# Performance work log

Measured on AMD Instinct MI355X. Metric: run time of the kernel, lower is better.

## Reference

```python
import jax, jax.numpy as jnp
import numpy as np

N_STEPS = 192
T_END = 8.0


def _forward(z, dec_W, dec_b, templates, def_W1, def_b1, def_W2, def_b2,
             al_W1, al_b1, al_W2, al_b2, ode_W1, ode_b1, ode_W2, ode_b2):
    B = z.shape[0]
    n_slots, crf_dim = templates.shape  # (32, 99)
    # vae.decoder: latent -> per-slot embeddings (B, 32, 64)
    slot_embs = (z @ dec_W + dec_b).reshape(B, n_slots, -1)
    # initialize_crf: template library + deformation MLP -> base CRF (B, 32, 99)
    h = jax.nn.relu(slot_embs @ def_W1 + def_b1)
    base_crf = templates[None, :, :] + (h @ def_W2 + def_b2)
    # aliveness MLP -> per-slot logits (B, 32)
    ah = jax.nn.relu(slot_embs @ al_W1 + al_b1)
    logits = (ah @ al_W2 + al_b2)[..., 0]
    alive = jax.nn.sigmoid(logits)
    # state combiner: gated CRF flattened + aliveness -> (B, 32*99 + 32) = (B, 3200)
    y0 = jnp.concatenate([(base_crf * alive[..., None]).reshape(B, -1), alive], axis=-1)

    dt = jnp.asarray(T_END / (N_STEPS - 1), y0.dtype)

    def f(y):  # ODEFx: autonomous 2-layer tanh MLP on the (B, 3200) state
        return jnp.tanh(y @ ode_W1 + ode_b1) @ ode_W2 + ode_b2

    def step(y, _):  # classic fixed-step RK4 (torchdiffeq method='rk4')
        k1 = f(y)
        k2 = f(y + 0.5 * dt * k1)
        k3 = f(y + 0.5 * dt * k2)
        k4 = f(y + dt * k3)
        yn = y + (dt / 6.0) * (k1 + 2.0 * k2 + 2.0 * k3 + k4)
        return yn, yn

    _, traj = jax.lax.scan(jax.checkpoint(step), y0, None, length=N_STEPS - 1)
    return jnp.concatenate([y0[None], traj], axis=0)  # (192, B, 3200)


def setup_inputs() -> dict:
    key = jax.random.key(0)
    ks = jax.random.split(key, 9)
    B, LAT, NS, SD, CRF, DH, OH, STATE = 128, 128, 32, 64, 99, 128, 4096, 3200
    r = lambda k, shp, fan: (jax.random.normal(k, shp, jnp.float32) / np.float32(np.sqrt(fan)))
    return dict(
        z=jax.random.normal(ks[0], (B, LAT), jnp.float32),
        dec_W=r(ks[1], (LAT, NS * SD), LAT), dec_b=jnp.zeros((NS * SD,), jnp.float32),
        templates=jax.random.normal(ks[2], (NS, CRF), jnp.float32),
        def_W1=r(ks[3], (SD, DH), SD), def_b1=jnp.zeros((DH,), jnp.float32),
        def_W2=r(ks[4], (DH, CRF), DH), def_b2=jnp.zeros((CRF,), jnp.float32),
        al_W1=r(ks[5], (SD, NS), SD), al_b1=jnp.zeros((NS,), jnp.float32),
        al_W2=r(ks[6], (NS, 1), NS), al_b2=jnp.zeros((1,), jnp.float32),
        ode_W1=r(ks[7], (STATE, OH), STATE), ode_b1=jnp.zeros((OH,), jnp.float32),
        ode_W2=r(ks[8], (OH, STATE), OH), ode_b2=jnp.zeros((STATE,), jnp.float32),
    )


def reference(z, dec_W, dec_b, templates, def_W1, def_b1, def_W2, def_b2,
              al_W1, al_b1, al_W2, al_b2, ode_W1, ode_b1, ode_W2, ode_b2):
    return _forward(z, dec_W, dec_b, templates, def_W1, def_b1, def_W2, def_b2,
                    al_W1, al_b1, al_W2, al_b2, ode_W1, ode_b1, ode_W2, ode_b2)
```

## Files before the change

### kernel.cpp

```cpp
#include <hip/hip_runtime.h>
#include <hip/hip_bf16.h>

typedef __bf16 v8bf __attribute__((ext_vector_type(8)));
typedef float  v4f  __attribute__((ext_vector_type(4)));

__device__ inline const __attribute__((address_space(1))) void* gcast(const void* p) {
    return (const __attribute__((address_space(1))) void*)p;
}
__device__ inline __attribute__((address_space(3))) void* scast(void* p) {
    return (__attribute__((address_space(3))) void*)p;
}

__device__ inline float fast_tanh(float x) {
    float e = __expf(2.0f * x);
    return 1.0f - 2.0f / (e + 1.0f);
}

__global__ __launch_bounds__(256) void se_kernel(const float* __restrict__ z,
                                                 const float* __restrict__ decW,
                                                 const float* __restrict__ decb,
                                                 float* __restrict__ SE) {
    __shared__ float zs[128];
    const int b = blockIdx.x, t = threadIdx.x;
    if (t < 128) zs[t] = z[b * 128 + t];
    __syncthreads();
    for (int c = t; c < 2048; c += 256) {
        float acc = decb[c];
        #pragma unroll 4
        for (int k = 0; k < 128; ++k) acc += zs[k] * decW[k * 2048 + c];
        SE[b * 2048 + c] = acc;
    }
}

__global__ __launch_bounds__(128) void init_kernel(
    const float* __restrict__ SE, const float* __restrict__ tmpl,
    const float* __restrict__ dW1, const float* __restrict__ db1,
    const float* __restrict__ dW2, const float* __restrict__ db2,
    const float* __restrict__ aW1, const float* __restrict__ ab1,
    const float* __restrict__ aW2, const float* __restrict__ ab2,
    float* __restrict__ y, __bf16* __restrict__ ybf, float* __restrict__ out0) {
    __shared__ float se[64];
    __shared__ float h[128];
    __shared__ float ah[32];
    __shared__ float alive;
    const int r = blockIdx.x, b = r >> 5, s = r & 31, t = threadIdx.x;
    if (t < 64) se[t] = SE[b * 2048 + s * 64 + t];
    __syncthreads();
    {
        float acc = db1[t];
        #pragma unroll 4
        for (int k = 0; k < 64; ++k) acc += se[k] * dW1[k * 128 + t];
        h[t] = fmaxf(acc, 0.0f);
    }
    if (t < 32) {
        float acc = ab1[t];
        #pragma unroll 4
        for (int k = 0; k < 64; ++k) acc += se[k] * aW1[k * 32 + t];
        ah[t] = fmaxf(acc, 0.0f);
    }
    __syncthreads();
    if (t == 0) {
        float lg = ab2[0];
        #pragma unroll
        for (int j = 0; j < 32; ++j) lg += ah[j] * aW2[j];
        alive = 1.0f / (1.0f + __expf(-lg));
    }
    __syncthreads();
    if (t < 99) {
        float acc = db2[t];
        #pragma unroll 4
        for (int j = 0; j < 128; ++j) acc += h[j] * dW2[j * 99 + t];
        float v = (tmpl[s * 99 + t] + acc) * alive;
        int idx = b * 3200 + s * 99 + t;
        y[idx] = v; ybf[idx] = (__bf16)v; out0[idx] = v;
    } else if (t == 99) {
        int idx = b * 3200 + 3168 + s;
        y[idx] = alive; ybf[idx] = (__bf16)alive; out0[idx] = alive;
    }
}

__global__ __launch_bounds__(256) void transpose_bf16(const float* __restrict__ W,
                                                      __bf16* __restrict__ WT,
                                                      int R, int C) {
    __shared__ float tile[32][33];
    const int tx = threadIdx.x & 31, ty = threadIdx.x >> 5;
    const int c0 = blockIdx.x * 32, r0 = blockIdx.y * 32;
    #pragma unroll
    for (int i = 0; i < 4; ++i)
        tile[ty + 8 * i][tx] = W[(long)(r0 + ty + 8 * i) * C + c0 + tx];
    __syncthreads();
    #pragma unroll
    for (int i = 0; i < 4; ++i)
        WT[(long)(c0 + ty + 8 * i) * R + r0 + tx] = (__bf16)tile[tx][ty + 8 * i];
}

__global__ __launch_bounds__(256, 2) void gemm_step(
    const __bf16* __restrict__ A, const __bf16* __restrict__ BT,
    const float* __restrict__ bias, int K, int nTiles, int mode, float cc, float dt6,
    __bf16* __restrict__ obf, float* __restrict__ y, float* __restrict__ S,
    float* __restrict__ traj) {
    __shared__ __attribute__((aligned(16))) __bf16 lds[4][2][4096];

    const int t = threadIdx.x;
    const int lane = t & 63, w = t >> 6, q = lane >> 4, c16 = lane & 15;

    const int g = blockIdx.x >> 5, rr = blockIdx.x & 31;
    const int nt = g * 8 + (rr & 7);
    const int mt = rr >> 3;
    if (nt >= nTiles) return;
    const int m0 = mt * 32, n0 = nt * 32;
    const int N = nTiles * 32;

    const int sr = t >> 4;
    const int scg = (t & 15) ^ sr;
    const __bf16* pA0 = A  + (long)(m0 + sr)      * K + scg * 8;
    const __bf16* pA1 = A  + (long)(m0 + sr + 16) * K + scg * 8;
    const __bf16* pB0 = BT + (long)(n0 + sr)      * K + scg * 8;
    const __bf16* pB1 = BT + (long)(n0 + sr + 16) * K + scg * 8;

    v4f acc0 = {0.f, 0.f, 0.f, 0.f};
    v4f acc1 = {0.f, 0.f, 0.f, 0.f};

    const int wn = w & 1, wk = w >> 1;
    const int rowA0 = c16, rowA1 = c16 + 16, rowB = wn * 16 + c16;
    const int swz = c16;
    const int cb = wk * 8;

    const int nIter = K >> 7;

#define STAGE(buf, koff) do { \
    __builtin_amdgcn_global_load_lds(gcast(pA0 + (koff)), scast(&lds[buf][0][t * 8]),         16, 0, 0); \
    __builtin_amdgcn_global_load_lds(gcast(pA1 + (koff)), scast(&lds[buf][0][(t + 256) * 8]), 16, 0, 0); \
    __builtin_amdgcn_global_load_lds(gcast(pB0 + (koff)), scast(&lds[buf][1][t * 8]),         16, 0, 0); \
    __builtin_amdgcn_global_load_lds(gcast(pB1 + (koff)), scast(&lds[buf][1][(t + 256) * 8]), 16, 0, 0); \
} while (0)

    STAGE(0, 0);
    if (nIter > 1) STAGE(1, 128);
    if (nIter > 2) STAGE(2, 256);

    for (int it = 0; it < nIter; ++it) {
        const int ahead = nIter - 1 - it;
        __builtin_amdgcn_sched_barrier(0);
        if (ahead >= 2)      asm volatile("s_waitcnt vmcnt(8)" ::: "memory");
        else if (ahead == 1) asm volatile("s_waitcnt vmcnt(4)" ::: "memory");
        else                 asm volatile("s_waitcnt vmcnt(0)" ::: "memory");
        __builtin_amdgcn_sched_barrier(0);
        __builtin_amdgcn_s_barrier();
        __builtin_amdgcn_sched_barrier(0);
        if (it + 3 < nIter) STAGE((it + 3) & 3, (it + 3) * 128);

        const __bf16* bufA = lds[it & 3][0];
        const __bf16* bufB = lds[it & 3][1];
        v8bf a00 = *(const v8bf*)&bufA[(rowA0 * 16 + ((cb + q)     ^ swz)) * 8];
        v8bf a10 = *(const v8bf*)&bufA[(rowA1 * 16 + ((cb + q)     ^ swz)) * 8];
        v8bf b0  = *(const v8bf*)&bufB[(rowB  * 16 + ((cb + q)     ^ swz)) * 8];
        v8bf a01 = *(const v8bf*)&bufA[(rowA0 * 16 + ((cb + 4 + q) ^ swz)) * 8];
        v8bf a11 = *(const v8bf*)&bufA[(rowA1 * 16 + ((cb + 4 + q) ^ swz)) * 8];
        v8bf b1  = *(const v8bf*)&bufB[(rowB  * 16 + ((cb + 4 + q) ^ swz)) * 8];
        __builtin_amdgcn_s_setprio(1);
        acc0 = __builtin_amdgcn_mfma_f32_16x16x32_bf16(a00, b0, acc0, 0, 0, 0);
        acc1 = __builtin_amdgcn_mfma_f32_16x16x32_bf16(a10, b0, acc1, 0, 0, 0);
        acc0 = __builtin_amdgcn_mfma_f32_16x16x32_bf16(a01, b1, acc0, 0, 0, 0);
        acc1 = __builtin_amdgcn_mfma_f32_16x16x32_bf16(a11, b1, acc1, 0, 0, 0);
        __builtin_amdgcn_s_setprio(0);
    }
#undef STAGE

    __syncthreads();
    float* red = (float*)&lds[0][0][0];
    if (wk == 1) {
        #pragma unroll
        for (int r = 0; r < 4; ++r) {
            red[r * 128 + wn * 64 + lane]       = acc0[r];
            red[(r + 4) * 128 + wn * 64 + lane] = acc1[r];
        }
    }
    __syncthreads();
    if (wk != 0) return;
    #pragma unroll
    for (int r = 0; r < 4; ++r) {
        acc0[r] += red[r * 128 + wn * 64 + lane];
        acc1[r] += red[(r + 4) * 128 + wn * 64 + lane];
    }

    const int gcol = n0 + 16 * wn + c16;
    const float b0s = bias[gcol];
    #pragma unroll
    for (int mA = 0; mA < 2; ++mA) {
        v4f acc = mA ? acc1 : acc0;
        #pragma unroll
        for (int r = 0; r < 4; ++r) {
            const int grow = m0 + 16 * mA + 4 * q + r;
            const float v = acc[r] + b0s;
            const long idx = (long)grow * N + gcol;
            if (mode == 0) {
                obf[idx] = (__bf16)fast_tanh(v);
            } else if (mode == 1) {
                S[idx] = v;
                obf[idx] = (__bf16)(y[idx] + cc * v);
            } else if (mode == 2) {
                S[idx] += 2.0f * v;
                obf[idx] = (__bf16)(y[idx] + cc * v);
            } else {
                float yn = y[idx] + dt6 * (S[idx] + v);
                y[idx] = yn;
                obf[idx] = (__bf16)yn;
                traj[idx] = yn;
            }
        }
    }
}

extern "C" void kernel_launch(void* const* d_in, const int* in_sizes, int n_in,
                              void* d_out, int out_size, void* d_ws, size_t ws_size,
                              hipStream_t stream) {
    const float* z     = (const float*)d_in[0];
    const float* decW  = (const float*)d_in[1];
    const float* decb  = (const float*)d_in[2];
    const float* tmpl  = (const float*)d_in[3];
    const float* dW1   = (const float*)d_in[4];
    const float* db1   = (const float*)d_in[5];
    const float* dW2   = (const float*)d_in[6];
    const float* db2   = (const float*)d_in[7];
    const float* aW1   = (const float*)d_in[8];
    const float* ab1   = (const float*)d_in[9];
    const float* aW2   = (const float*)d_in[10];
    const float* ab2   = (const float*)d_in[11];
    const float* odeW1 = (const float*)d_in[12];
    const float* odeb1 = (const float*)d_in[13];
    const float* odeW2 = (const float*)d_in[14];
    const float* odeb2 = (const float*)d_in[15];
    float* out = (float*)d_out;

    char* ws = (char*)d_ws;
    size_t off = 0;
    auto alloc = [&](size_t bytes) -> void* {
        void* p = ws + off;
        off = (off + bytes + 255) & ~(size_t)255;
        return p;
    };
    __bf16* w1t = (__bf16*)alloc((size_t)4096 * 3200 * 2);
    __bf16* w2t = (__bf16*)alloc((size_t)3200 * 4096 * 2);
    float*  SE  = (float*)alloc((size_t)128 * 2048 * 4);
    float*  yst = (float*)alloc((size_t)409600 * 4);
    float*  Sac = (float*)alloc((size_t)409600 * 4);
    __bf16* ybf = (__bf16*)alloc((size_t)409600 * 2);
    __bf16* hbf = (__bf16*)alloc((size_t)128 * 4096 * 2);

    transpose_bf16<<<dim3(128, 100), 256, 0, stream>>>(odeW1, w1t, 3200, 4096);
    transpose_bf16<<<dim3(100, 128), 256, 0, stream>>>(odeW2, w2t, 4096, 3200);
    se_kernel<<<128, 256, 0, stream>>>(z, decW, decb, SE);
    init_kernel<<<4096, 128, 0, stream>>>(SE, tmpl, dW1, db1, dW2, db2,
                                          aW1, ab1, aW2, ab2, yst, ybf, out);

    const float dt  = 8.0f / 191.0f;
    const float dt2 = 0.5f * dt;
    const float dt6 = dt / 6.0f;

    for (int s = 0; s < 191; ++s) {
        float* traj = out + (size_t)(s + 1) * 409600;
        gemm_step<<<512, 256, 0, stream>>>(ybf, w1t, odeb1, 3200, 128, 0, 0.f, 0.f,
                                           hbf, nullptr, nullptr, nullptr);
        gemm_step<<<416, 256, 0, stream>>>(hbf, w2t, odeb2, 4096, 100, 1, dt2, dt6,
                                           ybf, yst, Sac, nullptr);
        gemm_step<<<512, 256, 0, stream>>>(ybf, w1t, odeb1, 3200, 128, 0, 0.f, 0.f,
                                           hbf, nullptr, nullptr, nullptr);
        gemm_step<<<416, 256, 0, stream>>>(hbf, w2t, odeb2, 4096, 100, 2, dt2, dt6,
                                           ybf, yst, Sac, nullptr);
        gemm_step<<<512, 256, 0, stream>>>(ybf, w1t, odeb1, 3200, 128, 0, 0.f, 0.f,
                                           hbf, nullptr, nullptr, nullptr);
        gemm_step<<<416, 256, 0, stream>>>(hbf, w2t, odeb2, 4096, 100, 2, dt, dt6,
                                           ybf, yst, Sac, nullptr);
        gemm_step<<<512, 256, 0, stream>>>(ybf, w1t, odeb1, 3200, 128, 0, 0.f, 0.f,
                                           hbf, nullptr, nullptr, nullptr);
        gemm_step<<<416, 256, 0, stream>>>(hbf, w2t, odeb2, 4096, 100, 3, 0.f, dt6,
                                           ybf, yst, Sac, traj);
    }
}
```

Before: 22.98 ms.

## Use 32x32x16 MFMA with four-way split-K and LDS reduction in gemm_step

Replaces the per-wave pair of 16x16x32 MFMAs (two N-halves times two K-halves) with one 32x32x16 MFMA tile per wave. Each of the four waves now covers a different K slice of every 128-wide chunk. Partial accumulators from all four waves are reduced through LDS, and every wave then handles a quarter of the 32x32 output epilogue. This cuts LDS fragment loads per iteration from six to four and spreads the epilogue across all waves instead of two. In exchange it adds a four-way reduction step and larger accumulator registers.

Result: faster. 21.56 ms (-6.2%).

```diff
diff --git a/kernel.cpp b/kernel.cpp
--- a/kernel.cpp
+++ b/kernel.cpp
@@ -3,6 +3,7 @@
 
 typedef __bf16 v8bf __attribute__((ext_vector_type(8)));
 typedef float  v4f  __attribute__((ext_vector_type(4)));
+typedef float  v16f __attribute__((ext_vector_type(16)));
 
 __device__ inline const __attribute__((address_space(1))) void* gcast(const void* p) {
     return (const __attribute__((address_space(1))) void*)p;
@@ -102,7 +103,7 @@
     __shared__ __attribute__((aligned(16))) __bf16 lds[4][2][4096];
 
     const int t = threadIdx.x;
-    const int lane = t & 63, w = t >> 6, q = lane >> 4, c16 = lane & 15;
+    const int lane = t & 63, w = t >> 6;
 
     const int g = blockIdx.x >> 5, rr = blockIdx.x & 31;
     const int nt = g * 8 + (rr & 7);
@@ -118,13 +119,15 @@
     const __bf16* pB0 = BT + (long)(n0 + sr)      * K + scg * 8;
     const __bf16* pB1 = BT + (long)(n0 + sr + 16) * K + scg * 8;
 
-    v4f acc0 = {0.f, 0.f, 0.f, 0.f};
-    v4f acc1 = {0.f, 0.f, 0.f, 0.f};
-
-    const int wn = w & 1, wk = w >> 1;
-    const int rowA0 = c16, rowA1 = c16 + 16, rowB = wn * 16 + c16;
-    const int swz = c16;
-    const int cb = wk * 8;
+    v16f acc = {0.f, 0.f, 0.f, 0.f, 0.f, 0.f, 0.f, 0.f,
+                0.f, 0.f, 0.f, 0.f, 0.f, 0.f, 0.f, 0.f};
+
+    const int frow = lane & 31;
+    const int sw   = lane & 15;
+    const int cc0  = w * 4 + (lane >> 5);
+    const int cc1  = cc0 + 2;
+    const int off0 = (frow * 16 + (cc0 ^ sw)) * 8;
+    const int off1 = (frow * 16 + (cc1 ^ sw)) * 8;
 
     const int nIter = K >> 7;
 
@@ -152,62 +155,53 @@
 
         const __bf16* bufA = lds[it & 3][0];
         const __bf16* bufB = lds[it & 3][1];
-        v8bf a00 = *(const v8bf*)&bufA[(rowA0 * 16 + ((cb + q)     ^ swz)) * 8];
-        v8bf a10 = *(const v8bf*)&bufA[(rowA1 * 16 + ((cb + q)     ^ swz)) * 8];
-        v8bf b0  = *(const v8bf*)&bufB[(rowB  * 16 + ((cb + q)     ^ swz)) * 8];
-        v8bf a01 = *(const v8bf*)&bufA[(rowA0 * 16 + ((cb + 4 + q) ^ swz)) * 8];
-        v8bf a11 = *(const v8bf*)&bufA[(rowA1 * 16 + ((cb + 4 + q) ^ swz)) * 8];
-        v8bf b1  = *(const v8bf*)&bufB[(rowB  * 16 + ((cb + 4 + q) ^ swz)) * 8];
+        v8bf a0 = *(const v8bf*)&bufA[off0];
+        v8bf b0 = *(const v8bf*)&bufB[off0];
+        v8bf a1 = *(const v8bf*)&bufA[off1];
+        v8bf b1 = *(const v8bf*)&bufB[off1];
         __builtin_amdgcn_s_setprio(1);
-        acc0 = __builtin_amdgcn_mfma_f32_16x16x32_bf16(a00, b0, acc0, 0, 0, 0);
-        acc1 = __builtin_amdgcn_mfma_f32_16x16x32_bf16(a10, b0, acc1, 0, 0, 0);
-        acc0 = __builtin_amdgcn_mfma_f32_16x16x32_bf16(a01, b1, acc0, 0, 0, 0);
-        acc1 = __builtin_amdgcn_mfma_f32_16x16x32_bf16(a11, b1, acc1, 0, 0, 0);
+        acc = __builtin_amdgcn_mfma_f32_32x32x16_bf16(a0, b0, acc, 0, 0, 0);
+        acc = __builtin_amdgcn_mfma_f32_32x32x16_bf16(a1, b1, acc, 0, 0, 0);
         __builtin_amdgcn_s_setprio(0);
     }
 #undef STAGE
 
     __syncthreads();
     float* red = (float*)&lds[0][0][0];
-    if (wk == 1) {
-        #pragma unroll
-        for (int r = 0; r < 4; ++r) {
-            red[r * 128 + wn * 64 + lane]       = acc0[r];
-            red[(r + 4) * 128 + wn * 64 + lane] = acc1[r];
-        }
-    }
-    __syncthreads();
-    if (wk != 0) return;
-    #pragma unroll
-    for (int r = 0; r < 4; ++r) {
-        acc0[r] += red[r * 128 + wn * 64 + lane];
-        acc1[r] += red[(r + 4) * 128 + wn * 64 + lane];
-    }
-
-    const int gcol = n0 + 16 * wn + c16;
-    const float b0s = bias[gcol];
-    #pragma unroll
-    for (int mA = 0; mA < 2; ++mA) {
-        v4f acc = mA ? acc1 : acc0;
-        #pragma unroll
-        for (int r = 0; r < 4; ++r) {
-            const int grow = m0 + 16 * mA + 4 * q + r;
-            const float v = acc[r] + b0s;
-            const long idx = (long)grow * N + gcol;
-            if (mode == 0) {
-                obf[idx] = (__bf16)fast_tanh(v);
-            } else if (mode == 1) {
-                S[idx] = v;
-                obf[idx] = (__bf16)(y[idx] + cc * v);
-            } else if (mode == 2) {
-                S[idx] += 2.0f * v;
-                obf[idx] = (__bf16)(y[idx] + cc * v);
-            } else {
-                float yn = y[idx] + dt6 * (S[idx] + v);
-                y[idx] = yn;
-                obf[idx] = (__bf16)yn;
-                traj[idx] = yn;
-            }
+    #pragma unroll
+    for (int qq = 0; qq < 4; ++qq) {
+        v4f part = {acc[4 * qq + 0], acc[4 * qq + 1], acc[4 * qq + 2], acc[4 * qq + 3]};
+        *(v4f*)&red[((w * 4 + qq) * 64 + lane) * 4] = part;
+    }
+    __syncthreads();
+    v4f sum = {0.f, 0.f, 0.f, 0.f};
+    #pragma unroll
+    for (int ww = 0; ww < 4; ++ww) {
+        v4f p = *(const v4f*)&red[((ww * 4 + w) * 64 + lane) * 4];
+        sum += p;
+    }
+
+    const int gcol = n0 + (lane & 31);
+    const float bs = bias[gcol];
+    const int rbase = m0 + 8 * w + 4 * (lane >> 5);
+    #pragma unroll
+    for (int c = 0; c < 4; ++c) {
+        const int grow = rbase + c;
+        const float v = sum[c] + bs;
+        const long idx = (long)grow * N + gcol;
+        if (mode == 0) {
+            obf[idx] = (__bf16)fast_tanh(v);
+        } else if (mode == 1) {
+            S[idx] = v;
+            obf[idx] = (__bf16)(y[idx] + cc * v);
+        } else if (mode == 2) {
+            S[idx] += 2.0f * v;
+            obf[idx] = (__bf16)(y[idx] + cc * v);
+        } else {
+            float yn = y[idx] + dt6 * (S[idx] + v);
+            y[idx] = yn;
+            obf[idx] = (__bf16)yn;
+            traj[idx] = yn;
         }
     }
 }
```
